# Kernel tuning notes

Measured on AMD Instinct MI355X. Metric: run time of the kernel, lower is better.

The kernel has to match this reference:

```python
import jax, jax.numpy as jnp
import numpy as np

B, L, V, D, HD, T = 64, 512, 32000, 256, 512, 11
H = HD // 2  # per-direction hidden size
START_IDX, STOP_IDX = 9, 10


def setup_inputs() -> dict:
    key = jax.random.key(0)
    ks = jax.random.split(key, 14)
    s = 0.1
    emb = jax.random.normal(ks[0], (V, D)) * s
    W_ih_f = jax.random.normal(ks[1], (4 * H, D)) * s
    W_hh_f = jax.random.normal(ks[2], (4 * H, H)) * s
    b_f = jax.random.normal(ks[3], (4 * H,)) * s  # b_ih + b_hh fused
    W_ih_b = jax.random.normal(ks[4], (4 * H, D)) * s
    W_hh_b = jax.random.normal(ks[5], (4 * H, H)) * s
    b_b = jax.random.normal(ks[6], (4 * H,)) * s
    W_out = jax.random.normal(ks[7], (T, HD)) * s
    b_out = jnp.zeros((T,), jnp.float32)
    trans = jax.random.normal(ks[8], (T, T))
    trans = trans.at[:, START_IDX].set(-1000.0).at[STOP_IDX, :].set(-1000.0)
    h0 = jax.random.normal(ks[9], (2, B, H))  # init_hidden() uses randn
    c0 = jax.random.normal(ks[10], (2, B, H))
    sentences = jax.random.randint(ks[11], (B, L), 0, V, dtype=jnp.int32)
    return dict(sentences=sentences, emb=emb, W_ih_f=W_ih_f, W_hh_f=W_hh_f,
                b_f=b_f, W_ih_b=W_ih_b, W_hh_b=W_hh_b, b_b=b_b,
                W_out=W_out, b_out=b_out, trans=trans, h0=h0, c0=c0)


def _lstm_dir(x, h0, c0, W_ih, W_hh, b):
    # x: [B, L, D]; PyTorch gate order i, f, g, o
    def step(carry, x_t):
        h, c = carry
        g = x_t @ W_ih.T + h @ W_hh.T + b
        i, f, gg, o = jnp.split(g, 4, axis=-1)
        c = jax.nn.sigmoid(f) * c + jax.nn.sigmoid(i) * jnp.tanh(gg)
        h = jax.nn.sigmoid(o) * jnp.tanh(c)
        return (h, c), h
    xs = jnp.swapaxes(x, 0, 1)  # [L, B, D]
    _, hs = jax.lax.scan(step, (h0, c0), xs)
    return jnp.swapaxes(hs, 0, 1)  # [B, L, H]


def reference(sentences, emb, W_ih_f, W_hh_f, b_f, W_ih_b, W_hh_b, b_b,
              W_out, b_out, trans, h0, c0):
    x = emb[sentences]  # [B, L, D]
    hf = _lstm_dir(x, h0[0], c0[0], W_ih_f, W_hh_f, b_f)
    hb = _lstm_dir(x[:, ::-1], h0[1], c0[1], W_ih_b, W_hh_b, b_b)[:, ::-1]
    logits = jnp.concatenate([hf, hb], axis=-1) @ W_out.T + b_out  # [B, L, T]

    def viterbi(lg):  # lg: [L, T]
        def step(prev, lg_t):
            v = prev[:, None] + trans          # v[i, j] = score(prev=i) + trans[i->j]
            best = jnp.max(v, axis=0)
            bp = jnp.argmax(v, axis=0)
            return lg_t + best, bp
        last, bps = jax.lax.scan(step, lg[0], lg[1:])  # bps: [L-1, T]
        score = jnp.max(last)
        last_tag = jnp.argmax(last).astype(jnp.int32)
        def back(state, bp):
            prev = bp[state].astype(jnp.int32)
            return prev, prev
        _, path_head = jax.lax.scan(back, last_tag, bps, reverse=True)
        path = jnp.concatenate([path_head, last_tag[None]])  # [L]
        return score, path

    scores, paths = jax.vmap(viterbi)(logits)
    return scores, paths
```

## Files before the change

### kernel.cpp

```cpp
#include <hip/hip_runtime.h>
#include <cstdint>
#include <cstddef>
#include <cstring>

#define LSEQ 512
#define BATCH 64
#define DIM 256
#define HID 256
#define NTAG 11

typedef float vf4 __attribute__((ext_vector_type(4)));
typedef __bf16 bf16x8 __attribute__((ext_vector_type(8)));
typedef float f32x4 __attribute__((ext_vector_type(4)));
typedef _Float16 h2 __attribute__((ext_vector_type(2)));
typedef unsigned short u16;

static __device__ __forceinline__ float dot2_f16(unsigned int w, unsigned int h, float acc)
{
#if __has_builtin(__builtin_amdgcn_fdot2)
    return __builtin_amdgcn_fdot2(__builtin_bit_cast(h2, w),
                                  __builtin_bit_cast(h2, h), acc, false);
#else
    h2 a = __builtin_bit_cast(h2, w), b = __builtin_bit_cast(h2, h);
    acc = fmaf((float)a.x, (float)b.x, acc);
    return fmaf((float)a.y, (float)b.y, acc);
#endif
}

static __device__ __forceinline__ float fast_sig(float x)
{
#if __has_builtin(__builtin_amdgcn_exp2f) && __has_builtin(__builtin_amdgcn_rcpf)
    return __builtin_amdgcn_rcpf(1.f + __builtin_amdgcn_exp2f(x * -1.442695041f));
#else
    return 1.f / (1.f + expf(-x));
#endif
}
static __device__ __forceinline__ float fast_tanh(float x)
{
#if __has_builtin(__builtin_amdgcn_exp2f) && __has_builtin(__builtin_amdgcn_rcpf)
    return 1.f - 2.f * __builtin_amdgcn_rcpf(__builtin_amdgcn_exp2f(x * 2.885390082f) + 1.f);
#else
    return tanhf(x);
#endif
}

static __device__ __forceinline__ uint4 poll_load16(const unsigned int* p)
{
    uint4 v;
    asm volatile("global_load_dwordx4 %0, %1, off sc0 sc1\n"
                 "s_waitcnt vmcnt(0)"
                 : "=&v"(v) : "v"(p) : "memory");
    return v;
}

__global__ void __launch_bounds__(256) cvt_bf16(
    const float* __restrict__ src, u16* __restrict__ dst, int n4)
{
    int i = blockIdx.x * blockDim.x + threadIdx.x;
    const int stride = gridDim.x * blockDim.x;
    for (; i < n4; i += stride) {
        float4 f = ((const float4*)src)[i];
        ushort4 r;
        unsigned int u;
        u = __float_as_uint(f.x); u += 0x7FFFu + ((u >> 16) & 1u); r.x = (u16)(u >> 16);
        u = __float_as_uint(f.y); u += 0x7FFFu + ((u >> 16) & 1u); r.y = (u16)(u >> 16);
        u = __float_as_uint(f.z); u += 0x7FFFu + ((u >> 16) & 1u); r.z = (u16)(u >> 16);
        u = __float_as_uint(f.w); u += 0x7FFFu + ((u >> 16) & 1u); r.w = (u16)(u >> 16);
        ((ushort4*)dst)[i] = r;
    }
}

__global__ void __launch_bounds__(256) cvt_f16(
    const float* __restrict__ src, u16* __restrict__ dst, int n4)
{
    int i = blockIdx.x * blockDim.x + threadIdx.x;
    const int stride = gridDim.x * blockDim.x;
    for (; i < n4; i += stride) {
        float4 f = ((const float4*)src)[i];
        ushort4 r;
        r.x = __builtin_bit_cast(u16, (_Float16)f.x);
        r.y = __builtin_bit_cast(u16, (_Float16)f.y);
        r.z = __builtin_bit_cast(u16, (_Float16)f.z);
        r.w = __builtin_bit_cast(u16, (_Float16)f.w);
        ((ushort4*)dst)[i] = r;
    }
}

__global__ void __launch_bounds__(256) gemm_in(
    const int* __restrict__ sent, const u16* __restrict__ embb,
    const u16* __restrict__ w16f, const u16* __restrict__ w16b,
    const float* __restrict__ bf_, const float* __restrict__ bb_,
    u16* __restrict__ Gin, int t0, int CT)
{
    const int mtile = blockIdx.x, ntile = blockIdx.y, dir = blockIdx.z;
    const u16* __restrict__ W16 = dir ? w16b : w16f;
    const float* __restrict__ bias = dir ? bb_ : bf_;
    const int tid = threadIdx.x;
    const int wave = tid >> 6, lane = tid & 63;
    const int wm = wave & 1, wn = wave >> 1;

    __shared__ u16 Asm[128][40];
    __shared__ u16 Bsm[128][40];

    const int row = tid >> 1, half = tid & 1;
    const u16* ap;
    {
        int m_g = mtile * 128 + row;
        int tl = m_g >> 6, b = m_g & 63;
        int tg = t0 + tl;
        int tt = dir ? (LSEQ - 1 - tg) : tg;
        ap = embb + (size_t)sent[b * LSEQ + tt] * DIM;
    }
    const u16* bp = W16 + (size_t)(ntile * 128 + row) * DIM;

    f32x4 acc[4][4];
#pragma unroll
    for (int i = 0; i < 4; i++)
#pragma unroll
        for (int j = 0; j < 4; j++) acc[i][j] = (f32x4){0.f, 0.f, 0.f, 0.f};

    const int col = lane & 15, quad = lane >> 4;

    for (int ki = 0; ki < 8; ki++) {
        const int k0 = ki * 32;
        __syncthreads();
        {
            uint4 a0 = *(const uint4*)(ap + k0 + half * 16);
            uint4 a1 = *(const uint4*)(ap + k0 + half * 16 + 8);
            uint4 b0 = *(const uint4*)(bp + k0 + half * 16);
            uint4 b1 = *(const uint4*)(bp + k0 + half * 16 + 8);
            *(uint4*)&Asm[row][half * 16 + 0] = a0;
            *(uint4*)&Asm[row][half * 16 + 8] = a1;
            *(uint4*)&Bsm[row][half * 16 + 0] = b0;
            *(uint4*)&Bsm[row][half * 16 + 8] = b1;
        }
        __syncthreads();

        bf16x8 af[4], bg[4];
#pragma unroll
        for (int i = 0; i < 4; i++) {
            af[i] = *(const bf16x8*)&Asm[wm * 64 + i * 16 + col][quad * 8];
            bg[i] = *(const bf16x8*)&Bsm[wn * 64 + i * 16 + col][quad * 8];
        }
#pragma unroll
        for (int mt = 0; mt < 4; mt++)
#pragma unroll
            for (int nt = 0; nt < 4; nt++)
                acc[mt][nt] = __builtin_amdgcn_mfma_f32_16x16x32_bf16(
                    af[mt], bg[nt], acc[mt][nt], 0, 0, 0);
    }

#pragma unroll
    for (int nt = 0; nt < 4; nt++) {
        const int n_g = ntile * 128 + wn * 64 + nt * 16 + col;
        const float bv = bias[n_g];
        const int q = n_g >> 8, e = n_g & 255;
#pragma unroll
        for (int mt = 0; mt < 4; mt++)
#pragma unroll
            for (int r = 0; r < 4; r++) {
                const int m_g = mtile * 128 + wm * 64 + mt * 16 + quad * 4 + r;
                const int tl = m_g >> 6, b = m_g & 63;
                Gin[(((size_t)(dir * CT + tl) * 64 + b) * 256 + e) * 4 + q]
                    = __builtin_bit_cast(u16, (_Float16)(acc[mt][nt][r] + bv));
            }
    }
}

__global__ void __launch_bounds__(256, 1) lstm_rec(
    const u16* __restrict__ Gin,
    const u16* __restrict__ Whh16f, const u16* __restrict__ Whh16b,
    const float* __restrict__ h0, const float* __restrict__ c0,
    float* __restrict__ hs, unsigned int* __restrict__ htag,
    float* __restrict__ cbuf, int t0, int CT)
{
    const int wg = blockIdx.x;
    const int w = wg >> 5, g = wg & 31;
    const int dir   = g >> 4;
    const int bbase = (g & 15) << 2;
    const int tid = threadIdx.x;
    const int ks = tid & 15;
    const int ep = tid >> 4;
    const int ebase = w * 32 + ep * 2;
    const int P0 = ks & 1, P1 = (ks >> 1) & 1, P2 = (ks >> 2) & 1;
    const int bloc = ks & 3;
    const int e2sel = P2;
    const u16* __restrict__ Whh16 = dir ? Whh16b : Whh16f;

    __shared__ unsigned int Wl[256 * 65];
    __shared__ unsigned int Hd[2][4][132];

    const int wbase = tid * 65;

#pragma unroll
    for (int e2 = 0; e2 < 2; e2++)
#pragma unroll
        for (int q = 0; q < 4; q++) {
            const unsigned int* wp =
                (const unsigned int*)(Whh16 + (size_t)(q * 256 + ebase + e2) * HID);
#pragma unroll
            for (int j = 0; j < 2; j++) {
                *(uint4*)&Wl[wbase + ((e2 * 4 + q) * 2 + j) * 4] =
                    *(const uint4*)(wp + 8 * ks + 4 * j);
            }
        }

    float c = ((t0 == 0) ? c0 : cbuf)
        [((size_t)dir * BATCH + bbase + bloc) * HID + ebase + e2sel];

    const int sb = tid >> 6, k4 = tid & 63;

    const uint2* __restrict__ G2 = (const uint2*)Gin;
    const size_t gbase = (size_t)dir * CT * 16384
                       + (size_t)(bbase + bloc) * 256 + ebase + e2sel;
    uint2 gv = G2[gbase];

    __syncthreads();

    for (int t = t0; t < t0 + CT; t++) {
        const int wslot = t & 1;

        int tln = t + 1 - t0; if (tln >= CT) tln = CT - 1;
        const uint2 gvn = G2[gbase + (size_t)tln * 16384];

        {
            uint2 hp2;
            if (t == 0) {
                float4 hv = ((const float4*)(h0
                    + ((size_t)dir * BATCH + bbase + sb) * HID))[k4];
                hp2.x = __builtin_bit_cast(unsigned int,
                            (h2){(_Float16)hv.x, (_Float16)hv.y});
                hp2.y = __builtin_bit_cast(unsigned int,
                            (h2){(_Float16)hv.z, (_Float16)hv.w});
            } else {
                const unsigned int* hp =
                    htag + ((((size_t)((t - 1) & 1) * 2 + dir) * BATCH + bbase + sb) * HID
                            + 4 * k4);
                const unsigned int tg = (unsigned int)t;
                uint4 v;
                for (;;) {
                    v = poll_load16(hp);
                    if (((v.x >> 16) == tg) & ((v.y >> 16) == tg) &
                        ((v.z >> 16) == tg) & ((v.w >> 16) == tg))
                        break;
                    __builtin_amdgcn_s_sleep(1);
                }
                hp2.x = (v.x & 0xFFFFu) | (v.y << 16);
                hp2.y = (v.z & 0xFFFFu) | (v.w << 16);
            }
            *(uint2*)&Hd[wslot][sb][2 * k4] = hp2;
        }
        __syncthreads();

        float a[2][4][4];
#pragma unroll
        for (int e2 = 0; e2 < 2; e2++)
#pragma unroll
            for (int q = 0; q < 4; q++)
#pragma unroll
                for (int b = 0; b < 4; b++) a[e2][q][b] = 0.f;

#pragma unroll
        for (int i2 = 0; i2 < 2; i2++) {
            const int co = 8 * ks + 4 * i2;
            uint4 h4[4];
#pragma unroll
            for (int b = 0; b < 4; b++)
                h4[b] = *(const uint4*)&Hd[wslot][b][co];
#pragma unroll
            for (int e2 = 0; e2 < 2; e2++)
#pragma unroll
                for (int q = 0; q < 4; q++) {
                    const uint4 w4 =
                        *(const uint4*)&Wl[wbase + ((e2 * 4 + q) * 2 + i2) * 4];
#pragma unroll
                    for (int b = 0; b < 4; b++) {
                        a[e2][q][b] = dot2_f16(w4.x, h4[b].x, a[e2][q][b]);
                        a[e2][q][b] = dot2_f16(w4.y, h4[b].y, a[e2][q][b]);
                        a[e2][q][b] = dot2_f16(w4.z, h4[b].z, a[e2][q][b]);
                        a[e2][q][b] = dot2_f16(w4.w, h4[b].w, a[e2][q][b]);
                    }
                }
        }

        float gfin[4];
#pragma unroll
        for (int q = 0; q < 4; q++) {
            float m[2][2];
#pragma unroll
            for (int e2 = 0; e2 < 2; e2++) {
                float s01 = P0 ? a[e2][q][0] : a[e2][q][1];
                float s23 = P0 ? a[e2][q][2] : a[e2][q][3];
                m[e2][0] = (P0 ? a[e2][q][1] : a[e2][q][0]) + __shfl_xor(s01, 1, 64);
                m[e2][1] = (P0 ? a[e2][q][3] : a[e2][q][2]) + __shfl_xor(s23, 1, 64);
            }
            float gq[2];
#pragma unroll
            for (int e2 = 0; e2 < 2; e2++) {
                float s = P1 ? m[e2][0] : m[e2][1];
                gq[e2] = (P1 ? m[e2][1] : m[e2][0]) + __shfl_xor(s, 2, 64);
            }
            float s = P2 ? gq[0] : gq[1];
            float gk = (P2 ? gq[1] : gq[0]) + __shfl_xor(s, 4, 64);
            gk += __shfl_xor(gk, 8, 64);
            gfin[q] = gk;
        }

        const h2 g01 = __builtin_bit_cast(h2, gv.x);
        const h2 g23 = __builtin_bit_cast(h2, gv.y);
        const float x0 = gfin[0] + (float)g01.x;
        const float x1 = gfin[1] + (float)g01.y;
        const float x2 = gfin[2] + (float)g23.x;
        const float x3 = gfin[3] + (float)g23.y;
        c = fast_sig(x1) * c + fast_sig(x0) * fast_tanh(x2);
        const float h = fast_sig(x3) * fast_tanh(c);
        gv = gvn;

        if (ks < 8) {
            const int ee = ebase + e2sel;
            const int t_orig = dir ? (LSEQ - 1 - t) : t;
            const unsigned int pkt =
                ((unsigned int)(t + 1) << 16)
                | (unsigned int)__builtin_bit_cast(u16, (_Float16)h);
            __hip_atomic_store(
                &htag[(((size_t)wslot * 2 + dir) * BATCH + bbase + bloc) * HID + ee],
                pkt, __ATOMIC_RELAXED, __HIP_MEMORY_SCOPE_AGENT);
            hs[((size_t)(dir * LSEQ + t_orig) * BATCH + bbase + bloc) * HID + ee] = h;
        }
    }
    if (ks < 8)
        cbuf[((size_t)dir * BATCH + bbase + bloc) * HID + ebase + e2sel] = c;
}

__global__ void __launch_bounds__(256) logits_k(
    const float* __restrict__ hs, const float* __restrict__ Wout,
    const float* __restrict__ bout, float* __restrict__ logits)
{
    const int tid = threadIdx.x;
    const int rt = tid >> 4, tg = tid & 15;
    __shared__ float hrow[16][516];
    __shared__ float Wl[NTAG][516];
    const int rbase = blockIdx.x * 16;

#pragma unroll
    for (int i = 0; i < 8; i++) {
        int u  = tid + i * 256;
        int rr = u >> 7, c4 = u & 127;
        int r_g = rbase + rr;
        int b = r_g >> 9, t = r_g & 511;
        int d = (c4 >= 64) ? 1 : 0, k4 = c4 & 63;
        float4 hv = ((const float4*)hs)[(((size_t)d * LSEQ + t) * BATCH + b) * 64 + k4];
        *(float4*)&hrow[rr][c4 * 4] = hv;
    }
    for (int u = tid; u < NTAG * 128; u += 256) {
        int row = u >> 7, c4 = u & 127;
        float4 wv = ((const float4*)Wout)[(size_t)row * 128 + c4];
        *(float4*)&Wl[row][c4 * 4] = wv;
    }
    __syncthreads();

    if (tg < NTAG) {
        const float4* hp = (const float4*)&hrow[rt][0];
        const float4* wp = (const float4*)&Wl[tg][0];
        float acc = 0.f;
#pragma unroll 4
        for (int k = 0; k < 128; k++) {
            float4 h = hp[k], ww = wp[k];
            acc = fmaf(h.x, ww.x, acc); acc = fmaf(h.y, ww.y, acc);
            acc = fmaf(h.z, ww.z, acc); acc = fmaf(h.w, ww.w, acc);
        }
        int r_g = rbase + rt;
        logits[(size_t)r_g * NTAG + tg] = acc + bout[tg];
    }
}

__global__ void __launch_bounds__(64) viterbi_k(
    const float* __restrict__ logits, const float* __restrict__ trans,
    float* __restrict__ out)
{
    const int b = blockIdx.x, lane = threadIdx.x;
    __shared__ float lgl[LSEQ * NTAG];
    __shared__ unsigned char bp[LSEQ][16];
    __shared__ float pathf[LSEQ];

    {
        const float4* src = (const float4*)(logits + (size_t)b * LSEQ * NTAG);
        float4* dst = (float4*)lgl;
        for (int u = lane; u < (LSEQ * NTAG) / 4; u += 64) dst[u] = src[u];
    }
    float tcol[NTAG];
    if (lane < NTAG) {
#pragma unroll
        for (int i = 0; i < NTAG; i++) tcol[i] = trans[i * NTAG + lane];
    }
    __syncthreads();

    float v = (lane < NTAG) ? lgl[lane] : -1e30f;
    for (int t = 1; t < LSEQ; t++) {
        float best = -1e30f; int bi = 0;
#pragma unroll
        for (int i = 0; i < NTAG; i++) {
            float vi = __shfl(v, i, 64) + tcol[i];
            if (vi > best) { best = vi; bi = i; }
        }
        if (lane < NTAG) {
            v = lgl[t * NTAG + lane] + best;
            bp[t][lane] = (unsigned char)bi;
        }
    }
    float bestv = -1e30f; int bestj = 0;
#pragma unroll
    for (int j = 0; j < NTAG; j++) {
        float vj = __shfl(v, j, 64);
        if (vj > bestv) { bestv = vj; bestj = j; }
    }
    if (lane == 0) {
        out[b] = bestv;
        int st = bestj;
        pathf[LSEQ - 1] = (float)st;
        for (int t = LSEQ - 1; t >= 1; t--) { st = bp[t][st]; pathf[t - 1] = (float)st; }
    }
    __syncthreads();
    for (int t = lane; t < LSEQ; t += 64)
        out[BATCH + (size_t)b * LSEQ + t] = pathf[t];
}

extern "C" void kernel_launch(void* const* d_in, const int* in_sizes, int n_in,
                              void* d_out, int out_size, void* d_ws, size_t ws_size,
                              hipStream_t stream)
{
    (void)in_sizes; (void)n_in; (void)out_size;
    const int*   sent  = (const int*)  d_in[0];
    const float* emb   = (const float*)d_in[1];
    const float* Wihf  = (const float*)d_in[2];
    const float* Whhf  = (const float*)d_in[3];
    const float* bf    = (const float*)d_in[4];
    const float* Wihb  = (const float*)d_in[5];
    const float* Whhb  = (const float*)d_in[6];
    const float* bb    = (const float*)d_in[7];
    const float* Wout  = (const float*)d_in[8];
    const float* bout  = (const float*)d_in[9];
    const float* trans = (const float*)d_in[10];
    const float* h0    = (const float*)d_in[11];
    const float* c0    = (const float*)d_in[12];
    float* out = (float*)d_out;

    const size_t fixed = 16777216ull + 262144ull + 32768ull + 360448ull
                       + 4096000ull + 131072ull + 131072ull
                       + 131072ull + 131072ull;
    int CT = LSEQ;
    while (CT > 8 && ((size_t)CT * 65536ull + fixed) * 4ull > ws_size) CT >>= 1;

    float* ws = (float*)d_ws;
    size_t off = 0;
    u16* Gin = (u16*)(ws + off); off += (size_t)CT * 65536ull;
    float* hs   = ws + off; off += 16777216ull;
    unsigned int* htag = (unsigned int*)(ws + off); off += 262144ull;
    float* cbuf = ws + off; off += 32768ull;
    float* lgts = ws + off; off += 360448ull;
    u16* embb = (u16*)(ws + off); off += 4096000ull;
    u16* w16f = (u16*)(ws + off); off += 131072ull;
    u16* w16b = (u16*)(ws + off); off += 131072ull;
    u16* whh16f = (u16*)(ws + off); off += 131072ull;
    u16* whh16b = (u16*)(ws + off); off += 131072ull;

    hipLaunchKernelGGL(cvt_bf16, dim3(2048), dim3(256), 0, stream,
                       emb, embb, (32000 * 256) / 4);
    hipLaunchKernelGGL(cvt_bf16, dim3(256), dim3(256), 0, stream,
                       Wihf, w16f, (1024 * 256) / 4);
    hipLaunchKernelGGL(cvt_bf16, dim3(256), dim3(256), 0, stream,
                       Wihb, w16b, (1024 * 256) / 4);
    hipLaunchKernelGGL(cvt_f16, dim3(256), dim3(256), 0, stream,
                       Whhf, whh16f, (1024 * 256) / 4);
    hipLaunchKernelGGL(cvt_f16, dim3(256), dim3(256), 0, stream,
                       Whhb, whh16b, (1024 * 256) / 4);

    const int nch = LSEQ / CT;
    for (int c = 0; c < nch; c++) {
        int t0 = c * CT;
        hipLaunchKernelGGL(gemm_in, dim3(CT / 2, 8, 2), dim3(256), 0, stream,
                           sent, embb, w16f, w16b, bf, bb, Gin, t0, CT);
        hipLaunchKernelGGL(lstm_rec, dim3(256), dim3(256), 0, stream,
                           Gin, whh16f, whh16b, h0, c0, hs, htag, cbuf, t0, CT);
    }
    hipLaunchKernelGGL(logits_k, dim3((BATCH * LSEQ) / 16), dim3(256), 0, stream,
                       hs, Wout, bout, lgts);
    hipLaunchKernelGGL(viterbi_k, dim3(BATCH), dim3(64), 0, stream,
                       lgts, trans, out);
}
```

Before: 1.524 ms.

## Replace per-element tagged h polling with per-workgroup counters; stage full K in LDS

The recurrent kernel stops embedding a timestep tag in every hidden-state word. Each wave now bumps a per-group counter after its stores drain, and consumers poll eight counters before reading the plain h data. The aim is to cut the cost of the cross-workgroup handshake on the serial critical path. The input GEMM also loads the whole K=256 slice into LDS once, removing the per-k-step barriers at the cost of more shared memory. This relies on relaxed atomics plus a waitcnt for ordering, which could weaken memory-visibility guarantees.

```diff
diff --git a/kernel.cpp b/kernel.cpp
--- a/kernel.cpp
+++ b/kernel.cpp
@@ -99,8 +99,8 @@
     const int wave = tid >> 6, lane = tid & 63;
     const int wm = wave & 1, wn = wave >> 1;
 
-    __shared__ u16 Asm[128][40];
-    __shared__ u16 Bsm[128][40];
+    __shared__ u16 Asm[128][264];
+    __shared__ u16 Bsm[128][264];
 
     const int row = tid >> 1, half = tid & 1;
     const u16* ap;
@@ -113,6 +113,15 @@
     }
     const u16* bp = W16 + (size_t)(ntile * 128 + row) * DIM;
 
+#pragma unroll
+    for (int j = 0; j < 16; j++) {
+        *(uint4*)&Asm[row][half * 128 + j * 8] =
+            *(const uint4*)(ap + half * 128 + j * 8);
+        *(uint4*)&Bsm[row][half * 128 + j * 8] =
+            *(const uint4*)(bp + half * 128 + j * 8);
+    }
+    __syncthreads();
+
     f32x4 acc[4][4];
 #pragma unroll
     for (int i = 0; i < 4; i++)
@@ -121,26 +130,14 @@
 
     const int col = lane & 15, quad = lane >> 4;
 
+#pragma unroll
     for (int ki = 0; ki < 8; ki++) {
         const int k0 = ki * 32;
-        __syncthreads();
-        {
-            uint4 a0 = *(const uint4*)(ap + k0 + half * 16);
-            uint4 a1 = *(const uint4*)(ap + k0 + half * 16 + 8);
-            uint4 b0 = *(const uint4*)(bp + k0 + half * 16);
-            uint4 b1 = *(const uint4*)(bp + k0 + half * 16 + 8);
-            *(uint4*)&Asm[row][half * 16 + 0] = a0;
-            *(uint4*)&Asm[row][half * 16 + 8] = a1;
-            *(uint4*)&Bsm[row][half * 16 + 0] = b0;
-            *(uint4*)&Bsm[row][half * 16 + 8] = b1;
-        }
-        __syncthreads();
-
         bf16x8 af[4], bg[4];
 #pragma unroll
         for (int i = 0; i < 4; i++) {
-            af[i] = *(const bf16x8*)&Asm[wm * 64 + i * 16 + col][quad * 8];
-            bg[i] = *(const bf16x8*)&Bsm[wn * 64 + i * 16 + col][quad * 8];
+            af[i] = *(const bf16x8*)&Asm[wm * 64 + i * 16 + col][k0 + quad * 8];
+            bg[i] = *(const bf16x8*)&Bsm[wn * 64 + i * 16 + col][k0 + quad * 8];
         }
 #pragma unroll
         for (int mt = 0; mt < 4; mt++)
@@ -171,8 +168,9 @@
     const u16* __restrict__ Gin,
     const u16* __restrict__ Whh16f, const u16* __restrict__ Whh16b,
     const float* __restrict__ h0, const float* __restrict__ c0,
-    float* __restrict__ hs, unsigned int* __restrict__ htag,
-    float* __restrict__ cbuf, int t0, int CT)
+    float* __restrict__ hs, unsigned int* __restrict__ hdat,
+    unsigned int* __restrict__ hcnt, float* __restrict__ cbuf,
+    int t0, int CT)
 {
     const int wg = blockIdx.x;
     const int w = wg >> 5, g = wg & 31;
@@ -210,6 +208,11 @@
 
     const int sb = tid >> 6, k4 = tid & 63;
 
+    const unsigned int* __restrict__ cp =
+        hcnt + ((size_t)dir * 16 + (g & 15)) * 16;
+    unsigned int* __restrict__ mycnt =
+        hcnt + ((size_t)dir * 16 + (g & 15)) * 16 + w;
+
     const uint2* __restrict__ G2 = (const uint2*)Gin;
     const size_t gbase = (size_t)dir * CT * 16384
                        + (size_t)(bbase + bloc) * 256 + ebase + e2sel;
@@ -233,18 +236,19 @@
                 hp2.y = __builtin_bit_cast(unsigned int,
                             (h2){(_Float16)hv.z, (_Float16)hv.w});
             } else {
-                const unsigned int* hp =
-                    htag + ((((size_t)((t - 1) & 1) * 2 + dir) * BATCH + bbase + sb) * HID
-                            + 4 * k4);
-                const unsigned int tg = (unsigned int)t;
-                uint4 v;
+                const unsigned int tgt = 4u * (unsigned int)t;
                 for (;;) {
-                    v = poll_load16(hp);
-                    if (((v.x >> 16) == tg) & ((v.y >> 16) == tg) &
-                        ((v.z >> 16) == tg) & ((v.w >> 16) == tg))
+                    uint4 c0 = poll_load16(cp);
+                    uint4 c1 = poll_load16(cp + 4);
+                    if ((c0.x >= tgt) & (c0.y >= tgt) & (c0.z >= tgt) & (c0.w >= tgt) &
+                        (c1.x >= tgt) & (c1.y >= tgt) & (c1.z >= tgt) & (c1.w >= tgt))
                         break;
                     __builtin_amdgcn_s_sleep(1);
                 }
+                const unsigned int* dp = hdat
+                    + ((((size_t)((t - 1) & 1) * 2 + dir) * BATCH + bbase + sb) * HID
+                       + 4 * k4);
+                uint4 v = poll_load16(dp);
                 hp2.x = (v.x & 0xFFFFu) | (v.y << 16);
                 hp2.y = (v.z & 0xFFFFu) | (v.w << 16);
             }
@@ -320,13 +324,16 @@
             const int ee = ebase + e2sel;
             const int t_orig = dir ? (LSEQ - 1 - t) : t;
             const unsigned int pkt =
-                ((unsigned int)(t + 1) << 16)
-                | (unsigned int)__builtin_bit_cast(u16, (_Float16)h);
+                (unsigned int)__builtin_bit_cast(u16, (_Float16)h);
             __hip_atomic_store(
-                &htag[(((size_t)wslot * 2 + dir) * BATCH + bbase + bloc) * HID + ee],
+                &hdat[(((size_t)wslot * 2 + dir) * BATCH + bbase + bloc) * HID + ee],
                 pkt, __ATOMIC_RELAXED, __HIP_MEMORY_SCOPE_AGENT);
             hs[((size_t)(dir * LSEQ + t_orig) * BATCH + bbase + bloc) * HID + ee] = h;
         }
+        asm volatile("s_waitcnt vmcnt(0)" ::: "memory");
+        if ((tid & 63) == 0)
+            __hip_atomic_fetch_add(mycnt, 1u,
+                __ATOMIC_RELAXED, __HIP_MEMORY_SCOPE_AGENT);
     }
     if (ks < 8)
         cbuf[((size_t)dir * BATCH + bbase + bloc) * HID + ebase + e2sel] = c;
@@ -455,7 +462,9 @@
     size_t off = 0;
     u16* Gin = (u16*)(ws + off); off += (size_t)CT * 65536ull;
     float* hs   = ws + off; off += 16777216ull;
-    unsigned int* htag = (unsigned int*)(ws + off); off += 262144ull;
+    unsigned int* hdat = (unsigned int*)(ws + off);
+    unsigned int* hcnt = (unsigned int*)(ws + off) + 65536;
+    off += 262144ull;
     float* cbuf = ws + off; off += 32768ull;
     float* lgts = ws + off; off += 360448ull;
     u16* embb = (u16*)(ws + off); off += 4096000ull;
@@ -463,6 +472,8 @@
     u16* w16b = (u16*)(ws + off); off += 131072ull;
     u16* whh16f = (u16*)(ws + off); off += 131072ull;
     u16* whh16b = (u16*)(ws + off); off += 131072ull;
+
+    hipMemsetAsync(hcnt, 0, 32 * 16 * sizeof(unsigned int), stream);
 
     hipLaunchKernelGGL(cvt_bf16, dim3(2048), dim3(256), 0, stream,
                        emb, embb, (32000 * 256) / 4);
@@ -481,7 +492,8 @@
         hipLaunchKernelGGL(gemm_in, dim3(CT / 2, 8, 2), dim3(256), 0, stream,
                            sent, embb, w16f, w16b, bf, bb, Gin, t0, CT);
         hipLaunchKernelGGL(lstm_rec, dim3(256), dim3(256), 0, stream,
-                           Gin, whh16f, whh16b, h0, c0, hs, htag, cbuf, t0, CT);
+                           Gin, whh16f, whh16b, h0, c0, hs, hdat, hcnt, cbuf,
+                           t0, CT);
     }
     hipLaunchKernelGGL(logits_k, dim3((BATCH * LSEQ) / 16), dim3(256), 0, stream,
                        hs, Wout, bout, lgts);
```

Result: slower. 2.056 ms (+34.9%).
